# Performance work log

Hardware: AMD Instinct MI355X
Metric: run time of the kernel (lower is better)

Reference implementation:

```python
import jax, jax.numpy as jnp
import numpy as np
import math

N_NODES = 50000
N_EDGES = 800000
IN_DIM = 128
HID = 128
OUT_DIM = 2048
N_LABEL_EDGES = 4096
POOL_RATIO = 0.5
NUM_HEADS = 8


def seg_sum(x, idx, n):
    return jax.ops.segment_sum(x, idx, num_segments=n)


def graph_conv(x, W, b, src, dst, emask, n):
    # DGL GraphConv, norm='both': D_out^-1/2 A D_in^-1/2 (x W) + b (masked edges)
    deg_out = seg_sum(emask, src, n)
    deg_in = seg_sum(emask, dst, n)
    ns = jax.lax.rsqrt(jnp.maximum(deg_out, 1.0))
    nd = jax.lax.rsqrt(jnp.maximum(deg_in, 1.0))
    h = x @ W
    msg = (h * ns[:, None])[src] * emask[:, None]
    agg = seg_sum(msg, dst, n)
    return agg * nd[:, None] + b


def conv_pool_block(x, src, dst, emask, cW, cb, sW, sb):
    # GraphConv -> ReLU -> SAGPool(top-k by GraphConv score, tanh gate) -> avg||max readout
    n = x.shape[0]
    h = jax.nn.relu(graph_conv(x, cW, cb, src, dst, emask, n))
    score = graph_conv(h, sW, sb, src, dst, emask, n)[:, 0]
    k = int(math.ceil(POOL_RATIO * n))  # static
    _, perm = jax.lax.top_k(score, k)
    h_new = h[perm] * jnp.tanh(score[perm])[:, None]
    # remap edges to the pooled node set; drop edges touching removed nodes via mask
    newid = jnp.full((n,), -1, jnp.int32).at[perm].set(jnp.arange(k, dtype=jnp.int32))
    nsrc = newid[src]
    ndst = newid[dst]
    new_mask = emask * (nsrc >= 0).astype(emask.dtype) * (ndst >= 0).astype(emask.dtype)
    nsrc = jnp.maximum(nsrc, 0)
    ndst = jnp.maximum(ndst, 0)
    readout = jnp.concatenate([h_new.mean(0), h_new.max(0)])[None, :]  # [1, 2*HID]
    return h_new, nsrc, ndst, new_mask, readout


def gat_conv(x, fcW, al, ar, lsrc, ldst, n, slope=0.2):
    # GATConv(1 -> 1, num_heads=8): head feature dim is 1
    h = x @ fcW                      # [n, heads]
    el = h * al
    er = h * ar
    e = jax.nn.leaky_relu(el[lsrc] + er[ldst], slope)  # [E_l, heads]
    emax = jax.ops.segment_max(e, ldst, num_segments=n)
    emax = jnp.where(jnp.isfinite(emax), emax, 0.0)
    ex = jnp.exp(e - emax[ldst])
    denom = seg_sum(ex, ldst, n)
    alpha = ex / jnp.maximum(denom[ldst], 1e-9)
    out = seg_sum(alpha * h[lsrc], ldst, n)            # [n, heads]
    return out[:, :, None]                             # [n, heads, 1]


def setup_inputs() -> dict:
    key = jax.random.key(0)
    ks = jax.random.split(key, 32)

    def rn(k, shape, s=0.05):
        return jax.random.normal(k, shape, jnp.float32) * s

    inp = {}
    inp['feat'] = jax.random.normal(ks[0], (N_NODES, IN_DIM), jnp.float32)
    inp['sequence_feature'] = jax.random.normal(ks[1], (1, 1024), jnp.float32)
    inp['src'] = jax.random.randint(ks[2], (N_EDGES,), 0, N_NODES, jnp.int32)
    inp['dst'] = jax.random.randint(ks[3], (N_EDGES,), 0, N_NODES, jnp.int32)
    inp['label_src'] = jax.random.randint(ks[4], (N_LABEL_EDGES,), 0, OUT_DIM, jnp.int32)
    inp['label_dst'] = jax.random.randint(ks[5], (N_LABEL_EDGES,), 0, OUT_DIM, jnp.int32)
    i = 6
    for b in range(3):
        din = IN_DIM if b == 0 else HID
        inp['cW%d' % b] = rn(ks[i], (din, HID)); i += 1
        inp['cb%d' % b] = jnp.zeros((HID,), jnp.float32)
        inp['sW%d' % b] = rn(ks[i], (HID, 1)); i += 1
        inp['sb%d' % b] = jnp.zeros((1,), jnp.float32)
    inp['lin1W'] = rn(ks[i], (2 * HID + 1024, 2 * HID)); i += 1
    inp['lin1b'] = jnp.zeros((2 * HID,), jnp.float32)
    inp['lin2W'] = rn(ks[i], (2 * HID, HID)); i += 1
    inp['lin2b'] = jnp.zeros((HID,), jnp.float32)
    inp['lin3W'] = rn(ks[i], (HID, OUT_DIM)); i += 1
    inp['lin3b'] = jnp.zeros((OUT_DIM,), jnp.float32)
    inp['gat_fcW'] = rn(ks[i], (1, NUM_HEADS)); i += 1
    inp['gat_al'] = rn(ks[i], (NUM_HEADS,)); i += 1
    inp['gat_ar'] = rn(ks[i], (NUM_HEADS,)); i += 1
    return inp


def reference(feat, sequence_feature, src, dst, label_src, label_dst,
              cW0, cb0, sW0, sb0, cW1, cb1, sW1, sb1, cW2, cb2, sW2, sb2,
              lin1W, lin1b, lin2W, lin2b, lin3W, lin3b,
              gat_fcW, gat_al, gat_ar):
    x, s, d = feat, src, dst
    emask = jnp.ones((src.shape[0],), jnp.float32)
    final = None
    for cW, cb, sW, sb in ((cW0, cb0, sW0, sb0), (cW1, cb1, sW1, sb1), (cW2, cb2, sW2, sb2)):
        x, s, d, emask, ro = conv_pool_block(x, s, d, emask, cW, cb, sW, sb)
        final = ro if final is None else final + ro
    final = jnp.concatenate([final, sequence_feature], axis=-1)  # [1, 2*HID+1024]
    f = jax.nn.relu(final @ lin1W + lin1b)
    # dropout: eval mode -> identity
    f = jax.nn.relu(f @ lin2W + lin2b)
    f = f @ lin3W + lin3b          # [1, OUT_DIM]
    ft = f.T                       # [OUT_DIM, 1]
    gat_out = gat_conv(ft, gat_fcW, gat_al, gat_ar, label_src, label_dst, OUT_DIM)
    max_value = jnp.max(gat_out, axis=1)      # [OUT_DIM, 1]
    _ = ft - jax.nn.relu(max_value)           # computed then discarded, as in source
    return ft.T
```

## Files before the change

kernel.cpp:

```cpp
#include <hip/hip_runtime.h>
#include <hip/hip_bf16.h>
#include <cmath>

#define N0 50000
#define NEDGE 800000
#define NEG_HUGE -3.402823466e38f
#define STRIDE 128
#define HBINS 12500
#define HSLICE 16

typedef int i32x4 __attribute__((ext_vector_type(4)));
typedef __attribute__((ext_vector_type(8))) short short8v;
typedef __attribute__((ext_vector_type(4))) float f32x4;

__device__ inline float b2f(unsigned short u) { return __uint_as_float(((unsigned)u) << 16); }

__device__ inline unsigned short f2b(float f) {
    __hip_bfloat16 h = __float2bfloat16(f);
    return *(unsigned short*)&h;
}

__device__ inline unsigned fkey(float f) {
    unsigned b = __float_as_uint(f);
    if (b == 0x80000000u) b = 0u;
    return (b & 0x80000000u) ? ~b : (b | 0x80000000u);
}

__device__ inline void atomicMaxF(float* a, float v) {
    if (v >= 0.f) atomicMax((int*)a, __float_as_int(v));
    else          atomicMin((unsigned int*)a, __float_as_uint(v));
}

__global__ void k_init(float* finalv, int* deg_out, int* fill,
                       int* binsA, int* binsB, float* maxbuf, int* ctrl) {
    int i = blockIdx.x * blockDim.x + threadIdx.x;
    if (i < 256) finalv[i] = 0.f;
    if (i < 384) maxbuf[i] = NEG_HUGE;
    if (i < N0) { deg_out[i] = 0; fill[i] = 0; }
    if (i < 65536) { binsA[i] = 0; binsB[i] = 0; }
    if (i < 2) ctrl[8 + i] = 0;
}

__global__ __launch_bounds__(1024) void k_hist(const int* __restrict__ esrc,
                                               unsigned* __restrict__ deg_part) {
    __shared__ unsigned hist[HBINS];
    int b = blockIdx.x;
    int r = b & 3;
    int slice = b >> 2;
    for (int i = threadIdx.x; i < HBINS; i += 1024) hist[i] = 0;
    __syncthreads();
    int lo = r * HBINS;
    int base = slice * (NEDGE / HSLICE);
    for (int e = threadIdx.x * 4; e < NEDGE / HSLICE; e += 4096) {
        i32x4 a = __builtin_nontemporal_load((const i32x4*)(esrc + base + e));
        int ss[4] = {a.x, a.y, a.z, a.w};
#pragma unroll
        for (int q = 0; q < 4; ++q) {
            unsigned loc = (unsigned)(ss[q] - lo);
            if (loc < (unsigned)HBINS) atomicAdd(&hist[loc], 1u);
        }
    }
    __syncthreads();
    for (int i = threadIdx.x; i < HBINS; i += 1024)
        deg_part[(size_t)slice * N0 + lo + i] = hist[i];
}

__global__ void k_dsum(const unsigned* __restrict__ deg_part, int* deg_out) {
    int v = blockIdx.x * 256 + threadIdx.x;
    if (v >= N0) return;
    unsigned s = 0;
#pragma unroll
    for (int q = 0; q < HSLICE; ++q) s += deg_part[(size_t)q * N0 + v];
    deg_out[v] = (int)s;
}

__global__ __launch_bounds__(256) void k_build(
        const int* __restrict__ esrc, const int* __restrict__ edst,
        int* fill, int* csr_src) {
    int t = blockIdx.x * 256 + threadIdx.x;
    int e0 = t * 4;
    if (e0 >= NEDGE) return;
    i32x4 a = __builtin_nontemporal_load((const i32x4*)(esrc + e0));
    i32x4 bq = __builtin_nontemporal_load((const i32x4*)(edst + e0));
    int s[4] = {a.x, a.y, a.z, a.w};
    int d[4] = {bq.x, bq.y, bq.z, bq.w};
#pragma unroll
    for (int kq = 0; kq < 4; ++kq) {
        int pos = atomicAdd(&fill[d[kq]], 1);
        if (pos < STRIDE) csr_src[(size_t)d[kq] * STRIDE + pos] = s[kq];
    }
}

__global__ __launch_bounds__(256) void k_rmbuild(
        const int* __restrict__ esrc, const int* __restrict__ edst,
        const int2* __restrict__ ein, int use_pair,
        const int* __restrict__ ctrl, int slot,
        const int* __restrict__ newid,
        int2* __restrict__ eout, int* __restrict__ outcnt,
        int* deg_out, int* fill, int* csr_src) {
    __shared__ int wbase[4];
    __shared__ int blkbase;
    int E = (slot < 0) ? NEDGE : ctrl[slot];
    if (blockIdx.x * 256 >= E) return;
    int i = blockIdx.x * 256 + threadIdx.x;
    int lane = threadIdx.x & 63, w = threadIdx.x >> 6;
    int ns = -1, nd = -1;
    if (i < E) {
        int s, d;
        if (use_pair) { int2 pr = ein[i]; s = pr.x; d = pr.y; }
        else { s = esrc[i]; d = edst[i]; }
        ns = newid[s]; nd = newid[d];
    }
    bool keep = (ns >= 0) && (nd >= 0);
    unsigned long long m = __ballot(keep);
    int rank = __popcll(m & ((1ull << lane) - 1ull));
    if (lane == 0) wbase[w] = __popcll(m);
    __syncthreads();
    if (threadIdx.x == 0)
        blkbase = atomicAdd(outcnt, wbase[0] + wbase[1] + wbase[2] + wbase[3]);
    __syncthreads();
    int base = blkbase;
    for (int q = 0; q < w; ++q) base += wbase[q];
    if (keep) {
        eout[base + rank] = make_int2(ns, nd);
        atomicAdd(&deg_out[ns], 1);
        int pos = atomicAdd(&fill[nd], 1);
        if (pos < STRIDE) csr_src[(size_t)nd * STRIDE + pos] = ns;
    }
}

__global__ __launch_bounds__(256) void k_gemm(
        const float* __restrict__ feat, const float* __restrict__ xprev,
        const int* __restrict__ oldid, const float* __restrict__ garr,
        const int* __restrict__ deg_out,
        const float* __restrict__ W, unsigned short* __restrict__ hpre,
        int n, int nprev, int mode) {
    __shared__ short Wt[128][136];
    __shared__ short Xt[64][136];
    __shared__ int ridx_s[64];
    __shared__ float esc_s[64];
    int tid = threadIdx.x;
    int r0 = blockIdx.x * 64;
    if (tid < 64) {
        int gr = r0 + tid;
        int ridx = 0; float esc = 0.f;
        if (gr < n) {
            if (mode == 0) {
                ridx = gr;
                esc = rsqrtf(fmaxf((float)deg_out[gr], 1.f));
            } else {
                int orow = oldid[gr];
                if ((unsigned)orow < (unsigned)nprev) {
                    ridx = orow;
                    esc = rsqrtf(fmaxf((float)deg_out[gr], 1.f)) * garr[gr];
                }
            }
        }
        ridx_s[tid] = ridx;
        esc_s[tid] = esc;
    }
    __syncthreads();
    {
        int col = tid & 127;
        int kh = tid >> 7;
#pragma unroll
        for (int c8 = 0; c8 < 8; ++c8) {
            int kb = kh * 64 + c8 * 8;
            unsigned short v[8];
#pragma unroll
            for (int j = 0; j < 8; ++j)
                v[j] = f2b(W[(size_t)(kb + j) * 128 + col]);
            *(uint4*)&Wt[col][kb] = *(uint4*)v;
        }
    }
    {
        const float* xsrc = (mode == 0) ? feat : xprev;
        int rr = tid >> 2;
        int kx = (tid & 3) * 32;
        const float4* xp = (const float4*)(xsrc + (size_t)ridx_s[rr] * 128 + kx);
#pragma unroll
        for (int c4 = 0; c4 < 8; ++c4) {
            float4 v = xp[c4];
            unsigned short u[4];
            u[0] = f2b(v.x); u[1] = f2b(v.y); u[2] = f2b(v.z); u[3] = f2b(v.w);
            *(uint2*)&Xt[rr][kx + c4 * 4] = *(uint2*)u;
        }
    }
    __syncthreads();

    int lane = tid & 63, w = tid >> 6;
    int row16 = lane & 15;
    int ko = (lane >> 4) * 8;
    f32x4 acc[8];
#pragma unroll
    for (int t = 0; t < 8; ++t) acc[t] = (f32x4){0.f, 0.f, 0.f, 0.f};
#pragma unroll
    for (int kc = 0; kc < 4; ++kc) {
        int kbase = kc * 32 + ko;
        short8v a = *(short8v*)&Xt[w * 16 + row16][kbase];
#pragma unroll
        for (int t = 0; t < 8; ++t) {
            short8v b = *(short8v*)&Wt[t * 16 + row16][kbase];
            acc[t] = __builtin_amdgcn_mfma_f32_16x16x32_bf16(a, b, acc[t], 0, 0, 0);
        }
    }
    int rq = (lane >> 4) * 4;
    float esc[4];
#pragma unroll
    for (int r = 0; r < 4; ++r) esc[r] = esc_s[w * 16 + rq + r];
#pragma unroll
    for (int r = 0; r < 4; ++r) {
        int gr = r0 + w * 16 + rq + r;
        if (gr < n) {
            unsigned short* op = hpre + (size_t)gr * 128;
#pragma unroll
            for (int t = 0; t < 8; ++t)
                op[t * 16 + (lane & 15)] = f2b(acc[t][r] * esc[r]);
        }
    }
}

__global__ __launch_bounds__(256) void k_agg_conv(
        const unsigned short* __restrict__ hpre, const int* __restrict__ fill,
        const int* __restrict__ deg_out,
        const int* __restrict__ csr_src,
        const float* __restrict__ cb, const float* __restrict__ sW,
        float* __restrict__ hpost, float* __restrict__ hs, int n) {
    int wid = threadIdx.x >> 6;
    int lane = threadIdx.x & 63;
    int d = blockIdx.x * 4 + wid;
    if (d >= n) return;
    int degin = fill[d];
    int cnt = min(degin, STRIDE);
    const int* bp = csr_src + (size_t)d * STRIDE;
    int half = lane >> 5;
    int l32 = lane & 31;
    float a0 = 0.f, a1 = 0.f, a2 = 0.f, a3 = 0.f;
    int j = 0;
    for (; j + 8 <= cnt; j += 8) {
        int s0 = bp[j + half];
        int s1 = bp[j + 2 + half];
        int s2 = bp[j + 4 + half];
        int s3 = bp[j + 6 + half];
        ushort4 u0 = ((const ushort4*)(hpre + (size_t)s0 * 128))[l32];
        ushort4 u1 = ((const ushort4*)(hpre + (size_t)s1 * 128))[l32];
        ushort4 u2 = ((const ushort4*)(hpre + (size_t)s2 * 128))[l32];
        ushort4 u3 = ((const ushort4*)(hpre + (size_t)s3 * 128))[l32];
        a0 += (b2f(u0.x) + b2f(u1.x)) + (b2f(u2.x) + b2f(u3.x));
        a1 += (b2f(u0.y) + b2f(u1.y)) + (b2f(u2.y) + b2f(u3.y));
        a2 += (b2f(u0.z) + b2f(u1.z)) + (b2f(u2.z) + b2f(u3.z));
        a3 += (b2f(u0.w) + b2f(u1.w)) + (b2f(u2.w) + b2f(u3.w));
    }
    for (; j < cnt; j += 2) {
        int jj = j + half;
        if (jj < cnt) {
            int s0 = bp[jj];
            ushort4 u0 = ((const ushort4*)(hpre + (size_t)s0 * 128))[l32];
            a0 += b2f(u0.x); a1 += b2f(u0.y); a2 += b2f(u0.z); a3 += b2f(u0.w);
        }
    }
    a0 += __shfl_xor(a0, 32);
    a1 += __shfl_xor(a1, 32);
    a2 += __shfl_xor(a2, 32);
    a3 += __shfl_xor(a3, 32);
    float nd2 = rsqrtf(fmaxf((float)degin, 1.f));
    int c0 = l32 * 4;
    float h0 = fmaxf(fmaf(a0, nd2, cb[c0]), 0.f);
    float h1 = fmaxf(fmaf(a1, nd2, cb[c0 + 1]), 0.f);
    float h2 = fmaxf(fmaf(a2, nd2, cb[c0 + 2]), 0.f);
    float h3 = fmaxf(fmaf(a3, nd2, cb[c0 + 3]), 0.f);
    if (half == 0)
        ((float4*)(hpost + (size_t)d * 128))[l32] = make_float4(h0, h1, h2, h3);
    float v = h0 * sW[c0] + h1 * sW[c0 + 1] + h2 * sW[c0 + 2] + h3 * sW[c0 + 3];
#pragma unroll
    for (int off = 16; off; off >>= 1) v += __shfl_down(v, off);
    if (lane == 0) hs[d] = v * rsqrtf(fmaxf((float)deg_out[d], 1.f));
}

__global__ void k_score_hist(const float* __restrict__ hs, const int* __restrict__ fill,
                             const int* __restrict__ csr_src,
                             const float* __restrict__ sb, float* score,
                             int* binsA, int n) {
    int d = blockIdx.x * blockDim.x + threadIdx.x;
    if (d >= n) return;
    int degin = fill[d];
    int cnt = min(degin, STRIDE);
    const int* bp = csr_src + (size_t)d * STRIDE;
    float sum = 0.f;
    int j = 0;
    for (; j + 8 <= cnt; j += 8) {
        int4 s0 = *(const int4*)(bp + j);
        int4 s1 = *(const int4*)(bp + j + 4);
        sum += ((hs[s0.x] + hs[s0.y]) + (hs[s0.z] + hs[s0.w])) +
               ((hs[s1.x] + hs[s1.y]) + (hs[s1.z] + hs[s1.w]));
    }
    for (; j + 4 <= cnt; j += 4) {
        int4 ss = *(const int4*)(bp + j);
        sum += (hs[ss.x] + hs[ss.y]) + (hs[ss.z] + hs[ss.w]);
    }
    for (; j < cnt; ++j) sum += hs[bp[j]];
    float sc = rsqrtf(fmaxf((float)degin, 1.f)) * sum + sb[0];
    score[d] = sc;
    atomicAdd(&binsA[fkey(sc) >> 16], 1);
}

__global__ void k_rhist2(const float* __restrict__ score, const int* __restrict__ ctrl,
                         int n, int* binsB) {
    unsigned p16 = (unsigned)ctrl[3];
    for (int i = blockIdx.x * 256 + threadIdx.x; i < n; i += gridDim.x * 256) {
        unsigned u = fkey(score[i]);
        if ((u >> 16) == p16) atomicAdd(&binsB[u & 0xFFFFu], 1);
    }
}

__global__ void k_rpick(int stage, int k0, int* ctrl, const int* __restrict__ bins) {
    __shared__ int gs[64];
    __shared__ int arr[1024];
    __shared__ int wsum[16];
    __shared__ int sChunk, sKrem;
    int t = threadIdx.x;
    {
        int c = t >> 4, sub = t & 15;
        const int4* p4 = (const int4*)(bins + (size_t)c * 1024);
        int s = 0;
#pragma unroll
        for (int q = 0; q < 16; ++q) {
            int4 v = p4[q * 16 + sub];
            s += v.x + v.y + v.z + v.w;
        }
#pragma unroll
        for (int off = 8; off; off >>= 1) s += __shfl_down(s, off, 16);
        if (sub == 0) gs[c] = s;
    }
    __syncthreads();
    if (t == 0) {
        int kneed = (stage == 0) ? k0 : ctrl[4];
        int cum = 0, c = 63;
        for (; c >= 1; --c) { int v = gs[c]; if (cum + v >= kneed) break; cum += v; }
        sChunk = c; sKrem = kneed - cum;
    }
    __syncthreads();
    int c = sChunk;
    int v = bins[(size_t)c * 1024 + t];
    arr[t] = v;
    int lane = t & 63, w = t >> 6;
    int s = v;
#pragma unroll
    for (int off = 32; off; off >>= 1) s += __shfl_down(s, off);
    if (lane == 0) wsum[w] = s;
    __syncthreads();
    if (t == 0) {
        int kneed = sKrem;
        int cum = 0, w2 = 15;
        for (; w2 >= 1; --w2) { int vv = wsum[w2]; if (cum + vv >= kneed) break; cum += vv; }
        int j = 63;
        for (; j >= 1; --j) { int vv = arr[w2 * 64 + j]; if (cum + vv >= kneed) break; cum += vv; }
        int bin = c * 1024 + w2 * 64 + j;
        if (stage == 0) { ctrl[3] = bin; ctrl[4] = kneed - cum; }
        else {
            ctrl[0] = (int)((((unsigned)ctrl[3]) << 16) | (unsigned)bin);
            ctrl[2] = kneed - cum;
        }
    }
}

__global__ __launch_bounds__(1024) void k_cemit2(
        const float* __restrict__ score, const int* __restrict__ ctrl,
        int n, int knext, int* newid, int* oldid, float* garr,
        int* deg_out, int* fill, int* binsA, int* binsB,
        const float* __restrict__ hpost, float* finalv, float* maxbuf, float invk) {
    __shared__ int wG[16], wE[16];
    __shared__ int redCG[16], redCE[16];
    __shared__ int selIdx[1024];
    __shared__ float selG[1024];
    __shared__ int selCnt;
    __shared__ float redS[1024], redM[1024];
    int b = blockIdx.x, tid = threadIdx.x;
    int lane = tid & 63, wv = tid >> 6;
    unsigned T = (unsigned)ctrl[0];
    int needEq = ctrl[2];

    if (knext > 0) {
        int gt = b * 1024 + tid, nt = gridDim.x * 1024;
        for (int z = gt; z < 65536; z += nt) { binsA[z] = 0; binsB[z] = 0; }
        for (int z = gt; z < knext; z += nt) { deg_out[z] = 0; fill[z] = 0; }
    }

    int cg_ = 0, ce_ = 0;
    int end = b << 10;
    for (int i = tid; i < end; i += 1024) {
        unsigned u = fkey(score[i]);
        cg_ += (u > T);
        ce_ += (u == T);
    }
#pragma unroll
    for (int off = 32; off; off >>= 1) {
        cg_ += __shfl_down(cg_, off);
        ce_ += __shfl_down(ce_, off);
    }
    if (lane == 0) { redCG[wv] = cg_; redCE[wv] = ce_; }
    if (tid == 0) selCnt = 0;

    int i = (b << 10) + tid;
    bool inb = (i < n);
    float sc = inb ? score[i] : 0.f;
    unsigned u = inb ? fkey(sc) : 0u;
    bool isG = inb && (u > T);
    bool isE = inb && (u == T);
    unsigned long long mG = __ballot(isG);
    unsigned long long mE = __ballot(isE);
    if (lane == 0) { wG[wv] = __popcll(mG); wE[wv] = __popcll(mE); }
    __syncthreads();

    int sGoff = 0, sEoff = 0;
#pragma unroll
    for (int w = 0; w < 16; ++w) { sGoff += redCG[w]; sEoff += redCE[w]; }
    int gW = 0, eW = 0;
    for (int w = 0; w < wv; ++w) { gW += wG[w]; eW += wE[w]; }
    unsigned long long below = (1ull << lane) - 1ull;
    int Gb = sGoff + gW + __popcll(mG & below);
    int Eb = sEoff + eW + __popcll(mE & below);
    if (inb) {
        bool sel = isG || (isE && (Eb < needEq));
        if (sel) {
            int j = Gb + min(Eb, needEq);
            newid[i] = j;
            oldid[j] = i;
            float g = tanhf(sc);
            garr[j] = g;
            int p = atomicAdd(&selCnt, 1);
            selIdx[p] = i;
            selG[p] = g;
        } else {
            newid[i] = -1;
        }
    }
    __syncthreads();

    int m = selCnt;
    int grp = tid >> 7, c = tid & 127;
    float sum = 0.f, mx = NEG_HUGE;
    for (int r = grp; r < m; r += 8) {
        float v = hpost[(size_t)selIdx[r] * 128 + c] * selG[r];
        sum += v;
        mx = fmaxf(mx, v);
    }
    redS[tid] = sum;
    redM[tid] = mx;
    __syncthreads();
    if (tid < 128) {
        float s2 = 0.f, m2 = NEG_HUGE;
#pragma unroll
        for (int g2 = 0; g2 < 8; ++g2) {
            s2 += redS[g2 * 128 + tid];
            m2 = fmaxf(m2, redM[g2 * 128 + tid]);
        }
        atomicAdd(&finalv[tid], s2 * invk);
        atomicMaxF(&maxbuf[tid], m2);
    }
}

__global__ __launch_bounds__(1024) void k_mlp(
        const float* __restrict__ finalv, const float* __restrict__ maxbuf,
        const float* __restrict__ seq,
        const float* __restrict__ W1, const float* __restrict__ b1,
        const float* __restrict__ W2, const float* __restrict__ b2,
        const float* __restrict__ W3, const float* __restrict__ b3,
        float* out) {
    __shared__ float fv[1280];
    __shared__ float part[1024];
    __shared__ float f1s[256];
    __shared__ float f2s[128];
    int tid = threadIdx.x;
    for (int j = tid; j < 1280; j += 1024) {
        float v;
        if (j < 128) v = finalv[j];
        else if (j < 256) v = maxbuf[j - 128] + maxbuf[j] + maxbuf[j + 128];
        else v = seq[j - 256];
        fv[j] = v;
    }
    __syncthreads();
    {
        int o = tid & 255, pr = tid >> 8;
        float acc = 0.f;
        for (int j = pr * 320; j < (pr + 1) * 320; ++j)
            acc = fmaf(fv[j], W1[(size_t)j * 256 + o], acc);
        part[tid] = acc;
    }
    __syncthreads();
    if (tid < 256) {
        float a = part[tid] + part[tid + 256] + part[tid + 512] + part[tid + 768];
        f1s[tid] = fmaxf(a + b1[tid], 0.f);
    }
    __syncthreads();
    {
        int o = tid & 127, pr = tid >> 7;
        float acc = 0.f;
        for (int j = pr * 32; j < (pr + 1) * 32; ++j)
            acc = fmaf(f1s[j], W2[(size_t)j * 128 + o], acc);
        part[tid] = acc;
    }
    __syncthreads();
    if (tid < 128) {
        float a = 0.f;
#pragma unroll
        for (int q = 0; q < 8; ++q) a += part[q * 128 + tid];
        f2s[tid] = fmaxf(a + b2[tid], 0.f);
    }
    __syncthreads();
    for (int col = tid; col < 2048; col += 1024) {
        float acc = 0.f;
#pragma unroll 4
        for (int j = 0; j < 128; ++j)
            acc = fmaf(f2s[j], W3[(size_t)j * 2048 + col], acc);
        out[col] = acc + b3[col];
    }
}

extern "C" void kernel_launch(void* const* d_in, const int* in_sizes, int n_in,
                              void* d_out, int out_size, void* d_ws, size_t ws_size,
                              hipStream_t stream) {
    (void)in_sizes; (void)n_in; (void)out_size; (void)ws_size;
    const float* feat = (const float*)d_in[0];
    const float* seq  = (const float*)d_in[1];
    const int* src = (const int*)d_in[2];
    const int* dst = (const int*)d_in[3];
    const float *cW[3], *cb[3], *sW[3], *sb[3];
    for (int b = 0; b < 3; ++b) {
        cW[b] = (const float*)d_in[6 + 4 * b];
        cb[b] = (const float*)d_in[7 + 4 * b];
        sW[b] = (const float*)d_in[8 + 4 * b];
        sb[b] = (const float*)d_in[9 + 4 * b];
    }
    const float* lin1W = (const float*)d_in[18];
    const float* lin1b = (const float*)d_in[19];
    const float* lin2W = (const float*)d_in[20];
    const float* lin2b = (const float*)d_in[21];
    const float* lin3W = (const float*)d_in[22];
    const float* lin3b = (const float*)d_in[23];
    float* out = (float*)d_out;

    char* p = (char*)d_ws;
    size_t off = 0;
    auto alloc = [&](size_t bytes) -> void* {
        void* r = p + off;
        off = (off + bytes + 255) & ~(size_t)255;
        return r;
    };
    unsigned short* hpre = (unsigned short*)alloc((size_t)N0 * 128 * 2);
    float* hpost  = (float*)alloc((size_t)N0 * 128 * 4);
    float* hs     = (float*)alloc((size_t)N0 * 4);
    float* score  = (float*)alloc((size_t)N0 * 4);
    int* deg_out  = (int*)alloc((size_t)N0 * 4);
    int* fill     = (int*)alloc((size_t)N0 * 4);
    unsigned* deg_part = (unsigned*)alloc((size_t)HSLICE * N0 * 4);
    int2* epair1  = (int2*)alloc((size_t)NEDGE * 8);
    int* csr_src  = (int*)alloc((size_t)N0 * STRIDE * 4);
    int* newid    = (int*)alloc((size_t)N0 * 4);
    int* oldid    = (int*)alloc((size_t)25000 * 4);
    float* garr   = (float*)alloc((size_t)25000 * 4);
    float* maxbuf = (float*)alloc(3 * 128 * 4);
    float* finalv = (float*)alloc(256 * 4);
    int* ctrl     = (int*)alloc(64 * 4);
    int* binsA    = (int*)alloc(65536 * 4);
    int* binsB    = (int*)alloc(65536 * 4);
    int2* epair2  = (int2*)hpre;

    const int nb[3] = {50000, 25000, 12500};
    const int kb[3] = {25000, 12500, 6250};

    k_init<<<256, 256, 0, stream>>>(finalv, deg_out, fill, binsA, binsB, maxbuf, ctrl);

    for (int b = 0; b < 3; ++b) {
        int n = nb[b], k = kb[b];
        int B = (n + 1023) / 1024;
        if (b == 0) {
            k_hist<<<64, 1024, 0, stream>>>(src, deg_part);
            k_dsum<<<(N0 + 255) / 256, 256, 0, stream>>>(deg_part, deg_out);
            k_build<<<(NEDGE / 4 + 255) / 256, 256, 0, stream>>>(src, dst, fill, csr_src);
        } else if (b == 1) {
            k_rmbuild<<<(NEDGE + 255) / 256, 256, 0, stream>>>(
                src, dst, (const int2*)0, 0, ctrl, -1, newid, epair1, ctrl + 8,
                deg_out, fill, csr_src);
        } else {
            k_rmbuild<<<(NEDGE + 255) / 256, 256, 0, stream>>>(
                (const int*)0, (const int*)0, epair1, 1, ctrl, 8, newid, epair2, ctrl + 9,
                deg_out, fill, csr_src);
        }
        k_gemm<<<(n + 63) / 64, 256, 0, stream>>>(feat, hpost, oldid, garr, deg_out, cW[b],
                                                  hpre, n, (b > 0) ? nb[b - 1] : 1,
                                                  (b == 0) ? 0 : 1);
        k_agg_conv<<<(n + 3) / 4, 256, 0, stream>>>(hpre, fill, deg_out, csr_src, cb[b],
                                                    sW[b], hpost, hs, n);
        k_score_hist<<<(n + 255) / 256, 256, 0, stream>>>(hs, fill, csr_src, sb[b],
                                                          score, binsA, n);
        k_rpick<<<1, 1024, 0, stream>>>(0, k, ctrl, binsA);
        k_rhist2<<<128, 256, 0, stream>>>(score, ctrl, n, binsB);
        k_rpick<<<1, 1024, 0, stream>>>(1, k, ctrl, binsB);
        k_cemit2<<<B, 1024, 0, stream>>>(score, ctrl, n, (b < 2) ? kb[b] : 0,
                                         newid, oldid, garr, deg_out, fill, binsA, binsB,
                                         hpost, finalv, maxbuf + b * 128,
                                         1.0f / (float)k);
    }

    k_mlp<<<1, 1024, 0, stream>>>(finalv, maxbuf, seq, lin1W, lin1b, lin2W, lin2b,
                                  lin3W, lin3b, out);
}
```

Measured before the change: 582.0 us.

## Split single-block MLP head into three multi-block kernels

Replaces the one-block fused MLP kernel with three kernels. Layer 1 is split over 10 blocks that combine partial sums with atomics, layer 2 runs in one block, and layer 3 is spread over 16 blocks. The aim is to stop streaming the weight matrices through a single compute unit and spread that load across many. In exchange it adds two extra kernel launches and atomic accumulation, which needs an extra zeroed buffer.

```diff
diff --git a/kernel.cpp b/kernel.cpp
--- a/kernel.cpp
+++ b/kernel.cpp
@@ -31,10 +31,10 @@
     else          atomicMin((unsigned int*)a, __float_as_uint(v));
 }
 
-__global__ void k_init(float* finalv, int* deg_out, int* fill,
+__global__ void k_init(float* finalv, float* f1raw, int* deg_out, int* fill,
                        int* binsA, int* binsB, float* maxbuf, int* ctrl) {
     int i = blockIdx.x * blockDim.x + threadIdx.x;
-    if (i < 256) finalv[i] = 0.f;
+    if (i < 256) { finalv[i] = 0.f; f1raw[i] = 0.f; }
     if (i < 384) maxbuf[i] = NEG_HUGE;
     if (i < N0) { deg_out[i] = 0; fill[i] = 0; }
     if (i < 65536) { binsA[i] = 0; binsB[i] = 0; }
@@ -460,61 +460,48 @@
     }
 }
 
-__global__ __launch_bounds__(1024) void k_mlp(
-        const float* __restrict__ finalv, const float* __restrict__ maxbuf,
-        const float* __restrict__ seq,
-        const float* __restrict__ W1, const float* __restrict__ b1,
-        const float* __restrict__ W2, const float* __restrict__ b2,
-        const float* __restrict__ W3, const float* __restrict__ b3,
-        float* out) {
-    __shared__ float fv[1280];
-    __shared__ float part[1024];
+__global__ void k_mlp1(const float* __restrict__ finalv, const float* __restrict__ maxbuf,
+                       const float* __restrict__ seq, const float* __restrict__ W1,
+                       float* f1raw) {
+    int o = threadIdx.x;
+    int j0 = blockIdx.x * 128;
+    float acc = 0.f;
+    for (int jj = 0; jj < 128; ++jj) {
+        int j = j0 + jj;
+        float fv;
+        if (j < 128) fv = finalv[j];
+        else if (j < 256) fv = maxbuf[j - 128] + maxbuf[j] + maxbuf[j + 128];
+        else fv = seq[j - 256];
+        acc = fmaf(fv, W1[(size_t)j * 256 + o], acc);
+    }
+    atomicAdd(&f1raw[o], acc);
+}
+
+__global__ void k_mlp2(const float* __restrict__ f1raw, const float* __restrict__ b1,
+                       const float* __restrict__ W2, const float* __restrict__ bb2,
+                       float* f2v) {
     __shared__ float f1s[256];
+    int t = threadIdx.x;
+    f1s[t] = fmaxf(f1raw[t] + b1[t], 0.f);
+    f1s[t + 128] = fmaxf(f1raw[t + 128] + b1[t + 128], 0.f);
+    __syncthreads();
+    float acc = 0.f;
+    for (int j = 0; j < 256; ++j)
+        acc = fmaf(f1s[j], W2[(size_t)j * 128 + t], acc);
+    f2v[t] = fmaxf(acc + bb2[t], 0.f);
+}
+
+__global__ void k_mlp3(const float* __restrict__ f2v, const float* __restrict__ W3,
+                       const float* __restrict__ b3, float* out) {
     __shared__ float f2s[128];
-    int tid = threadIdx.x;
-    for (int j = tid; j < 1280; j += 1024) {
-        float v;
-        if (j < 128) v = finalv[j];
-        else if (j < 256) v = maxbuf[j - 128] + maxbuf[j] + maxbuf[j + 128];
-        else v = seq[j - 256];
-        fv[j] = v;
-    }
-    __syncthreads();
-    {
-        int o = tid & 255, pr = tid >> 8;
-        float acc = 0.f;
-        for (int j = pr * 320; j < (pr + 1) * 320; ++j)
-            acc = fmaf(fv[j], W1[(size_t)j * 256 + o], acc);
-        part[tid] = acc;
-    }
-    __syncthreads();
-    if (tid < 256) {
-        float a = part[tid] + part[tid + 256] + part[tid + 512] + part[tid + 768];
-        f1s[tid] = fmaxf(a + b1[tid], 0.f);
-    }
-    __syncthreads();
-    {
-        int o = tid & 127, pr = tid >> 7;
-        float acc = 0.f;
-        for (int j = pr * 32; j < (pr + 1) * 32; ++j)
-            acc = fmaf(f1s[j], W2[(size_t)j * 128 + o], acc);
-        part[tid] = acc;
-    }
-    __syncthreads();
-    if (tid < 128) {
-        float a = 0.f;
-#pragma unroll
-        for (int q = 0; q < 8; ++q) a += part[q * 128 + tid];
-        f2s[tid] = fmaxf(a + b2[tid], 0.f);
-    }
-    __syncthreads();
-    for (int col = tid; col < 2048; col += 1024) {
-        float acc = 0.f;
-#pragma unroll 4
-        for (int j = 0; j < 128; ++j)
-            acc = fmaf(f2s[j], W3[(size_t)j * 2048 + col], acc);
-        out[col] = acc + b3[col];
-    }
+    int t = threadIdx.x;
+    f2s[t] = f2v[t];
+    __syncthreads();
+    int col = blockIdx.x * 128 + t;
+    float acc = 0.f;
+    for (int j = 0; j < 128; ++j)
+        acc = fmaf(f2s[j], W3[(size_t)j * 2048 + col], acc);
+    out[col] = acc + b3[col];
 }
 
 extern "C" void kernel_launch(void* const* d_in, const int* in_sizes, int n_in,
@@ -561,6 +548,8 @@
     float* garr   = (float*)alloc((size_t)25000 * 4);
     float* maxbuf = (float*)alloc(3 * 128 * 4);
     float* finalv = (float*)alloc(256 * 4);
+    float* f1raw  = (float*)alloc(256 * 4);
+    float* f2v    = (float*)alloc(128 * 4);
     int* ctrl     = (int*)alloc(64 * 4);
     int* binsA    = (int*)alloc(65536 * 4);
     int* binsB    = (int*)alloc(65536 * 4);
@@ -569,7 +558,8 @@
     const int nb[3] = {50000, 25000, 12500};
     const int kb[3] = {25000, 12500, 6250};
 
-    k_init<<<256, 256, 0, stream>>>(finalv, deg_out, fill, binsA, binsB, maxbuf, ctrl);
+    k_init<<<256, 256, 0, stream>>>(finalv, f1raw, deg_out, fill, binsA, binsB,
+                                    maxbuf, ctrl);
 
     for (int b = 0; b < 3; ++b) {
         int n = nb[b], k = kb[b];
@@ -603,6 +593,7 @@
                                          1.0f / (float)k);
     }
 
-    k_mlp<<<1, 1024, 0, stream>>>(finalv, maxbuf, seq, lin1W, lin1b, lin2W, lin2b,
-                                  lin3W, lin3b, out);
-}
+    k_mlp1<<<10, 256, 0, stream>>>(finalv, maxbuf, seq, lin1W, f1raw);
+    k_mlp2<<<1, 128, 0, stream>>>(f1raw, lin1b, lin2W, lin2b, f2v);
+    k_mlp3<<<16, 128, 0, stream>>>(f2v, lin3W, lin3b, out);
+}
```

Measured after the change: 573.2 us. No clear change (-1.5%).
